# Performance work log

Hardware: AMD Instinct MI355X
Metric: run time of the kernel (lower is better)

The kernel has to match this reference:

```python
import jax, jax.numpy as jnp
import numpy as np

B, S, DIM = 2, 2048, 2048
N_HEADS, N_KV_HEADS, HEAD_DIM = 16, 4, 128
ROPE_THETA = 10000.0
N_REP = N_HEADS // N_KV_HEADS


def make_freq_cis(seq_len, head_dim, theta):
    # (seq_len, head_dim//2, 2, 2) rotation matrices [[cos,-sin],[sin,cos]]
    freqs = 1.0 / (theta ** (np.arange(0, head_dim, 2, dtype=np.float32) / head_dim))
    t = np.arange(seq_len, dtype=np.float32)
    ang = np.outer(t, freqs)  # [S, head_dim//2]
    cos, sin = np.cos(ang), np.sin(ang)
    row0 = np.stack([cos, -sin], axis=-1)
    row1 = np.stack([sin, cos], axis=-1)
    return jnp.asarray(np.stack([row0, row1], axis=-2))  # [S, hd/2, 2, 2]


def setup_inputs() -> dict:
    key = jax.random.key(0)
    ks = jax.random.split(key, 5)
    std = DIM ** -0.5
    x = jax.random.normal(ks[0], (B, S, DIM), dtype=jnp.float32)
    wq = jax.random.normal(ks[1], (N_HEADS * HEAD_DIM, DIM), dtype=jnp.float32) * std
    wk = jax.random.normal(ks[2], (N_KV_HEADS * HEAD_DIM, DIM), dtype=jnp.float32) * std
    wv = jax.random.normal(ks[3], (N_KV_HEADS * HEAD_DIM, DIM), dtype=jnp.float32) * std
    wo = jax.random.normal(ks[4], (DIM, N_HEADS * HEAD_DIM), dtype=jnp.float32) * std
    freq_cis = make_freq_cis(S, HEAD_DIM, ROPE_THETA)
    return {"x": x, "freq_cis": freq_cis, "wq": wq, "wk": wk, "wv": wv, "wo": wo}


def apply_rotary(xh, fc):
    # xh: [B,S,H,hd]; fc: [S, hd/2, 2, 2]
    b, s, h, hd = xh.shape
    xr = xh.reshape(b, s, h, hd // 2, 2)
    out = jnp.einsum('bshdj,sdij->bshdi', xr, fc)
    return out.reshape(b, s, h, hd)


def attention_fwd(x, freq_cis, wq, wk, wv, wo):
    b, s, _ = x.shape
    xq = (x @ wq.T).reshape(b, s, N_HEADS, HEAD_DIM)
    xk = (x @ wk.T).reshape(b, s, N_KV_HEADS, HEAD_DIM)
    xv = (x @ wv.T).reshape(b, s, N_KV_HEADS, HEAD_DIM)
    xq = apply_rotary(xq, freq_cis[:s])
    xk = apply_rotary(xk, freq_cis[:s])
    # GQA repeat_kv (repeat_interleave along head dim)
    xk = jnp.repeat(xk, N_REP, axis=2)
    xv = jnp.repeat(xv, N_REP, axis=2)
    scale = HEAD_DIM ** -0.5
    scores = jnp.einsum('bqhd,bkhd->bhqk', xq, xk) * scale
    causal = jnp.tril(jnp.ones((s, s), dtype=bool))
    scores = jnp.where(causal[None, None], scores, jnp.float32(-1e30))
    probs = jax.nn.softmax(scores, axis=-1)
    out = jnp.einsum('bhqk,bkhd->bqhd', probs, xv).reshape(b, s, N_HEADS * HEAD_DIM)
    return out @ wo.T


def reference(x, freq_cis, wq, wk, wv, wo):
    return attention_fwd(x, freq_cis, wq, wk, wv, wo)
```

## Files before the change

kernel.cpp:

```cpp
#include <hip/hip_runtime.h>

#define S_LEN 2048
#define N_B 2
#define N_H 16
#define N_KVH 4
#define HD 128
#define LDQ 2048
#define LDK 1024

typedef __bf16 bf16x8 __attribute__((ext_vector_type(8)));
typedef float f32x4 __attribute__((ext_vector_type(4)));
typedef float f32x16 __attribute__((ext_vector_type(16)));
typedef int v2i __attribute__((ext_vector_type(2)));

__device__ __forceinline__ float bf2f(unsigned short u){
  unsigned int x = ((unsigned int)u) << 16; float f;
  __builtin_memcpy(&f, &x, 4); return f;
}
__device__ __forceinline__ unsigned short f2bf(float f){
  unsigned int x; __builtin_memcpy(&x, &f, 4);
  unsigned int r = x + 0x7fff + ((x >> 16) & 1);
  return (unsigned short)(r >> 16);
}
__device__ __forceinline__ unsigned int cvt_pk_bf16(float lo, float hi){
  unsigned int u;
  asm("v_cvt_pk_bf16_f32 %0, %1, %2" : "=v"(u) : "v"(lo), "v"(hi));
  return u;
}
__device__ __forceinline__ void gload16(const void* g, void* l){
  __builtin_amdgcn_global_load_lds((const __attribute__((address_space(1))) void*)g,
                                   (__attribute__((address_space(3))) void*)l, 16, 0, 0);
}

__global__ void cast_all(const float* __restrict__ x,  const float* __restrict__ wq,
                         const float* __restrict__ wk, const float* __restrict__ wv,
                         const float* __restrict__ wo, unsigned short* __restrict__ xb,
                         unsigned short* __restrict__ wqb, unsigned short* __restrict__ wkb,
                         unsigned short* __restrict__ wvb, unsigned short* __restrict__ wob){
  int i = blockIdx.x * 256 + threadIdx.x;
  const float* in; unsigned short* out; int j;
  if (i < 1048576)      { in = x;  out = xb;  j = i; }
  else if (i < 1572864) { in = wq; out = wqb; j = i - 1048576; }
  else if (i < 1703936) { in = wk; out = wkb; j = i - 1572864; }
  else if (i < 1835008) { in = wv; out = wvb; j = i - 1703936; }
  else                  { in = wo; out = wob; j = i - 1835008; }
  const float4* p = (const float4*)in + (size_t)j * 2;
  float4 a = p[0], b = p[1];
  uint4 o;
  o.x = (unsigned)f2bf(a.x) | ((unsigned)f2bf(a.y) << 16);
  o.y = (unsigned)f2bf(a.z) | ((unsigned)f2bf(a.w) << 16);
  o.z = (unsigned)f2bf(b.x) | ((unsigned)f2bf(b.y) << 16);
  o.w = (unsigned)f2bf(b.z) | ((unsigned)f2bf(b.w) << 16);
  ((uint4*)out)[j] = o;
}

__global__ void rope_kernel(unsigned short* __restrict__ X, const float* __restrict__ FC,
                            int cpr_log2, int ld_log2, int n8){
  int i = blockIdx.x * 256 + threadIdx.x;
  if (i >= n8) return;
  int row = i >> cpr_log2;
  int col = (i & ((1 << cpr_log2) - 1)) << 3;
  size_t idx = ((size_t)row << ld_log2) + col;
  int s = row & (S_LEN - 1);
  int d = col & (HD - 1);
  uint4 v = *(const uint4*)(X + idx);
  unsigned short* pv = (unsigned short*)&v;
  const float4* f4 = (const float4*)FC + ((size_t)s * 64 + (d >> 1));
  uint4 ov; unsigned short* po = (unsigned short*)&ov;
#pragma unroll
  for (int p = 0; p < 4; p++){
    float4 f = f4[p];
    float e = bf2f(pv[2*p]), o = bf2f(pv[2*p+1]);
    po[2*p]   = f2bf(f.x * e + f.y * o);
    po[2*p+1] = f2bf(f.z * e + f.w * o);
  }
  *(uint4*)(X + idx) = ov;
}

__global__ void transpose_v(const unsigned short* __restrict__ V, unsigned short* __restrict__ Vt, int ld){
  __shared__ unsigned short tile[32][33];
  int t = threadIdx.x;
  int s0 = blockIdx.x * 32;
  int c0 = blockIdx.y * 32;
  int r = t >> 3, cg = (t & 7) * 4;
  uint2 in2 = *(const uint2*)(V + (size_t)(s0 + r) * ld + c0 + cg);
  unsigned short* pi = (unsigned short*)&in2;
  tile[r][cg+0] = pi[0]; tile[r][cg+1] = pi[1]; tile[r][cg+2] = pi[2]; tile[r][cg+3] = pi[3];
  __syncthreads();
  int b = s0 >> 11, sl = s0 & (S_LEN - 1);
  int kvh = c0 >> 7, dd0 = c0 & (HD - 1);
  int dd = t >> 3, sg = (t & 7) * 4;
  uint2 o2; unsigned short* po = (unsigned short*)&o2;
  po[0] = tile[sg+0][dd]; po[1] = tile[sg+1][dd]; po[2] = tile[sg+2][dd]; po[3] = tile[sg+3][dd];
  *(uint2*)(Vt + (size_t)((b * N_KVH + kvh) * HD + dd0 + dd) * S_LEN + sl + sg) = o2;
}

__device__ __forceinline__ void storeC(float* C, size_t idx, float v){ C[idx] = v; }
__device__ __forceinline__ void storeC(unsigned short* C, size_t idx, float v){ C[idx] = f2bf(v); }

template <typename OutT>
__global__ __launch_bounds__(256, 2) void gemm_nt(const unsigned short* __restrict__ A,
                                                  const unsigned short* __restrict__ Bm,
                                                  OutT* __restrict__ C,
                                                  int M, int N, int K, int nbn){
  extern __shared__ char smem[];
  char* sA = smem; char* sB = smem + 16384;
  int bid = blockIdx.x;
  bid = (bid & 7) * (gridDim.x >> 3) + (bid >> 3);
  int bn = bid % nbn, bm = bid / nbn;
  int row0 = bm * 128, col0 = bn * 128;
  int t = threadIdx.x; int w = t >> 6, l = t & 63;
  int lr = l & 15, lg = l >> 4;
  int srow = t >> 3;
  int sg = (t & 7) ^ (srow & 7);
  const unsigned short* agp = A + (size_t)(row0 + srow) * K + sg * 8;
  const unsigned short* bgp = Bm + (size_t)(col0 + srow) * K + sg * 8;
  int wr = w >> 1, wc = w & 1;
  f32x4 acc[4][4] = {};
  for (int k0 = 0; k0 < K; k0 += 64){
    __syncthreads();
#pragma unroll
    for (int i = 0; i < 4; i++){
      gload16(agp + (size_t)i * 32 * K + k0, sA + i * 4096 + w * 1024);
      gload16(bgp + (size_t)i * 32 * K + k0, sB + i * 4096 + w * 1024);
    }
    __syncthreads();
#pragma unroll
    for (int kk = 0; kk < 2; kk++){
      bf16x8 af[4], bfv[4];
#pragma unroll
      for (int m = 0; m < 4; m++){
        int row = wr * 64 + m * 16 + lr;
        int kg = kk * 4 + lg;
        af[m] = *(const bf16x8*)(sA + row * 128 + ((kg ^ (row & 7)) << 4));
      }
#pragma unroll
      for (int n = 0; n < 4; n++){
        int row = wc * 64 + n * 16 + lr;
        int kg = kk * 4 + lg;
        bfv[n] = *(const bf16x8*)(sB + row * 128 + ((kg ^ (row & 7)) << 4));
      }
#pragma unroll
      for (int m = 0; m < 4; m++)
#pragma unroll
        for (int n = 0; n < 4; n++)
          acc[m][n] = __builtin_amdgcn_mfma_f32_16x16x32_bf16(af[m], bfv[n], acc[m][n], 0, 0, 0);
    }
  }
#pragma unroll
  for (int m = 0; m < 4; m++)
#pragma unroll
    for (int n = 0; n < 4; n++)
#pragma unroll
      for (int r = 0; r < 4; r++){
        int rr = row0 + wr * 64 + m * 16 + lg * 4 + r;
        int cc = col0 + wc * 64 + n * 16 + lr;
        storeC(C, (size_t)rr * N + cc, acc[m][n][r]);
      }
}

template <typename OutT>
__global__ __launch_bounds__(512, 2) void gemm_tpl(const unsigned short* __restrict__ A,
                                                   const unsigned short* __restrict__ Bm,
                                                   OutT* __restrict__ C,
                                                   int M, int N, int K, int nbn){
  extern __shared__ char smem[];
  int bid = blockIdx.x;
  bid = (bid & 7) * (gridDim.x >> 3) + (bid >> 3);
  int bn = bid % nbn, bm = bid / nbn;
  int row0 = bm * 128, col0 = bn * 256;
  int t = threadIdx.x, w = t >> 6, l = t & 63;
  int lr = l & 15, lg = l >> 4;
  int wm = w >> 2, wn = w & 3;
  int srow = t >> 3;
  int sg = (t & 7) ^ (srow & 7);
  const unsigned short* agp = A + (size_t)(row0 + srow) * K + sg * 8;
  const unsigned short* bgp = Bm + (size_t)(col0 + srow) * K + sg * 8;
  int nk = K >> 6;
  f32x4 acc[4][4] = {};

#define TPL_STAGE_H1(j, s) do {                                                \
    char* base_ = smem + (s) * 49152;                                          \
    int k0_ = (j) << 6;                                                        \
    _Pragma("unroll")                                                          \
    for (int i_ = 0; i_ < 2; i_++)                                             \
      gload16(agp + (size_t)i_ * 64 * K + k0_, base_ + i_ * 8192 + w * 1024);  \
    gload16(bgp + k0_, base_ + 16384 + w * 1024);                              \
  } while(0)
#define TPL_STAGE_H2(j, s) do {                                                \
    char* base_ = smem + (s) * 49152;                                          \
    int k0_ = (j) << 6;                                                        \
    _Pragma("unroll")                                                          \
    for (int i_ = 1; i_ < 4; i_++)                                             \
      gload16(bgp + (size_t)i_ * 64 * K + k0_, base_ + 16384 + i_ * 8192 + w * 1024); \
  } while(0)

  TPL_STAGE_H1(0, 0); TPL_STAGE_H2(0, 0);
  TPL_STAGE_H1(1, 1); TPL_STAGE_H2(1, 1);
  int slot = 0;
  for (int j = 0; j < nk; j++){
    if (j + 1 < nk) asm volatile("s_waitcnt vmcnt(6)" ::: "memory");
    else            asm volatile("s_waitcnt vmcnt(0)" ::: "memory");
    __builtin_amdgcn_s_barrier();
    asm volatile("" ::: "memory");
    char* sA = smem + slot * 49152;
    char* sB = sA + 16384;
    int sn = slot + 2; if (sn >= 3) sn -= 3;
    {
      bf16x8 af[4], bfv[4];
#pragma unroll
      for (int m = 0; m < 4; m++){
        int row = wm * 64 + m * 16 + lr;
        af[m] = *(const bf16x8*)(sA + row * 128 + ((lg ^ (row & 7)) << 4));
      }
#pragma unroll
      for (int n = 0; n < 4; n++){
        int row = wn * 64 + n * 16 + lr;
        bfv[n] = *(const bf16x8*)(sB + row * 128 + ((lg ^ (row & 7)) << 4));
      }
      if (j + 2 < nk) TPL_STAGE_H1(j + 2, sn);
      __builtin_amdgcn_s_barrier();
      __builtin_amdgcn_s_setprio(1);
#pragma unroll
      for (int m = 0; m < 4; m++)
#pragma unroll
        for (int n = 0; n < 4; n++)
          acc[m][n] = __builtin_amdgcn_mfma_f32_16x16x32_bf16(af[m], bfv[n], acc[m][n], 0, 0, 0);
      __builtin_amdgcn_s_setprio(0);
      __builtin_amdgcn_s_barrier();
    }
    {
      bf16x8 af[4], bfv[4];
#pragma unroll
      for (int m = 0; m < 4; m++){
        int row = wm * 64 + m * 16 + lr;
        int kg = 4 + lg;
        af[m] = *(const bf16x8*)(sA + row * 128 + ((kg ^ (row & 7)) << 4));
      }
#pragma unroll
      for (int n = 0; n < 4; n++){
        int row = wn * 64 + n * 16 + lr;
        int kg = 4 + lg;
        bfv[n] = *(const bf16x8*)(sB + row * 128 + ((kg ^ (row & 7)) << 4));
      }
      if (j + 2 < nk) TPL_STAGE_H2(j + 2, sn);
      __builtin_amdgcn_s_barrier();
      __builtin_amdgcn_s_setprio(1);
#pragma unroll
      for (int m = 0; m < 4; m++)
#pragma unroll
        for (int n = 0; n < 4; n++)
          acc[m][n] = __builtin_amdgcn_mfma_f32_16x16x32_bf16(af[m], bfv[n], acc[m][n], 0, 0, 0);
      __builtin_amdgcn_s_setprio(0);
    }
    slot++; if (slot == 3) slot = 0;
  }
#undef TPL_STAGE_H1
#undef TPL_STAGE_H2
#pragma unroll
  for (int m = 0; m < 4; m++)
#pragma unroll
    for (int n = 0; n < 4; n++)
#pragma unroll
      for (int r = 0; r < 4; r++){
        int rr = row0 + wm * 64 + m * 16 + lg * 4 + r;
        int cc = col0 + wn * 64 + n * 16 + lr;
        storeC(C, (size_t)rr * N + cc, acc[m][n][r]);
      }
}

__global__ __launch_bounds__(256, 2) void attn_fwd(const unsigned short* __restrict__ Q,
                                                   const unsigned short* __restrict__ Kb,
                                                   const unsigned short* __restrict__ Vt,
                                                   unsigned short* __restrict__ P0,
                                                   unsigned short* __restrict__ P1,
                                                   float2* __restrict__ ML){
  extern __shared__ char smem[];
  const float SOFT_C = 0.088388347648318447f * 1.4426950408889634f;
  const float THR_RAW = 62.0f;
  int bid = blockIdx.x;
  bid = ((bid & 7) << 6) | (bid >> 3);
  int slot = bid & 15, h = (bid >> 4) & 15, b = bid >> 8;
  int p = slot & 7, half = slot >> 3;
  int kvh = h >> 2;
  int t = threadIdx.x, w = t >> 6, l = t & 63;
  int lq = l & 31, lh = l >> 5;
  unsigned short* Pout = half ? P1 : P0;
  float2* mlb = ML + half * (N_B * S_LEN * N_H);

  const unsigned short* kgp = Kb + ((size_t)(b * S_LEN) + (t & 63)) * LDK + kvh * HD + (t >> 6) * 8;
  const unsigned short* vgp = Vt + ((size_t)((b * N_KVH + kvh) * HD) + (t & 127)) * S_LEN + (t >> 7) * 8;

  for (int phase = 0; phase < 2; phase++){
    int qt = phase ? (15 - p) : p;
    int q_lane = qt * 128 + w * 32 + lq;
    const unsigned short* qbase = Q + ((size_t)(b * S_LEN + q_lane)) * LDQ + h * HD + lh * 8;
    bf16x8 qf[8];
#pragma unroll
    for (int ks = 0; ks < 8; ks++)
      qf[ks] = *(const bf16x8*)(qbase + ks * 16);

    f32x16 o_acc[4] = {};
    float m_run = -1e4f, l_run = 0.f;
    int t_begin = half ? (qt + 1) : 0;
    int t_end   = half ? (2 * qt + 2) : (qt + 1);

    {
      int k0 = t_begin * 64;
#pragma unroll
      for (int i = 0; i < 4; i++){
        gload16(kgp + (size_t)k0 * LDK + i * 32, smem + i * 4096 + t * 16);
        gload16(vgp + k0 + i * 16, smem + 16384 + i * 4096 + t * 16);
      }
    }
    __syncthreads();

    int cur = 0;
    for (int tix = t_begin; tix < t_end; tix++){
      int k0 = tix * 64;
      char* kb = smem + (cur << 15);
      if (tix + 1 < t_end){
        char* nb = smem + ((cur ^ 1) << 15);
        int nk0 = k0 + 64;
#pragma unroll
        for (int i = 0; i < 4; i++){
          gload16(kgp + (size_t)nk0 * LDK + i * 32, nb + i * 4096 + t * 16);
          gload16(vgp + nk0 + i * 16, nb + 16384 + i * 4096 + t * 16);
        }
      }

      f32x16 sc[2] = {};
      __builtin_amdgcn_s_setprio(1);
#pragma unroll
      for (int ks = 0; ks < 8; ks++){
#pragma unroll
        for (int n = 0; n < 2; n++){
          bf16x8 kf = *(const bf16x8*)(kb + (ks * 2 + lh) * 1024 + n * 512 + lq * 16);
          sc[n] = __builtin_amdgcn_mfma_f32_32x32x16_bf16(kf, qf[ks], sc[n], 0, 0, 0);
        }
      }
      __builtin_amdgcn_s_setprio(0);
      if (tix >= 2 * qt){
#pragma unroll
        for (int n = 0; n < 2; n++)
#pragma unroll
          for (int reg = 0; reg < 16; reg++){
            int kv = k0 + n * 32 + (reg & 3) + 8 * (reg >> 2) + 4 * lh;
            if (kv > q_lane) sc[n][reg] = -1e30f;
          }
      }
      float tmax = sc[0][0];
#pragma unroll
      for (int n = 0; n < 2; n++)
#pragma unroll
        for (int reg = 0; reg < 16; reg++) tmax = fmaxf(tmax, sc[n][reg]);
      tmax = fmaxf(tmax, __shfl_xor(tmax, 32));
      if (!__all(tmax - m_run <= THR_RAW)){
        float nm = fmaxf(m_run, tmax);
        float rs = exp2f((m_run - nm) * SOFT_C);
        m_run = nm;
        l_run *= rs;
#pragma unroll
        for (int n = 0; n < 4; n++)
#pragma unroll
          for (int j = 0; j < 16; j++) o_acc[n][j] *= rs;
      }
      float lsum = 0.f;
#pragma unroll
      for (int n = 0; n < 2; n++)
#pragma unroll
        for (int reg = 0; reg < 16; reg++){
          float pv = exp2f((sc[n][reg] - m_run) * SOFT_C);
          sc[n][reg] = pv;
          lsum += pv;
        }
      lsum += __shfl_xor(lsum, 32);
      l_run += lsum;

      bf16x8 pb[4];
#pragma unroll
      for (int ks = 0; ks < 4; ks++){
        int n = ks >> 1;
        int R0 = (2 * ks) & 3, R1 = (2 * ks + 1) & 3;
        unsigned int WA0 = cvt_pk_bf16(sc[n][4 * R0 + 0], sc[n][4 * R0 + 1]);
        unsigned int WA1 = cvt_pk_bf16(sc[n][4 * R0 + 2], sc[n][4 * R0 + 3]);
        unsigned int WB0 = cvt_pk_bf16(sc[n][4 * R1 + 0], sc[n][4 * R1 + 1]);
        unsigned int WB1 = cvt_pk_bf16(sc[n][4 * R1 + 2], sc[n][4 * R1 + 3]);
        v2i s0 = __builtin_amdgcn_permlane32_swap((int)WA0, (int)WB0, false, false);
        v2i s1 = __builtin_amdgcn_permlane32_swap((int)WA1, (int)WB1, false, false);
        unsigned int pu[4] = {(unsigned int)s0.x, (unsigned int)s1.x,
                              (unsigned int)s0.y, (unsigned int)s1.y};
        pb[ks] = *(bf16x8*)pu;
      }
      __builtin_amdgcn_s_setprio(1);
#pragma unroll
      for (int n = 0; n < 4; n++){
#pragma unroll
        for (int ks = 0; ks < 4; ks++){
          bf16x8 vf = *(const bf16x8*)(kb + 16384 + (ks * 2 + lh) * 2048 + n * 512 + lq * 16);
          o_acc[n] = __builtin_amdgcn_mfma_f32_32x32x16_bf16(vf, pb[ks], o_acc[n], 0, 0, 0);
        }
      }
      __builtin_amdgcn_s_setprio(0);
      __syncthreads();
      cur ^= 1;
    }
    unsigned short* ob = Pout + ((size_t)(b * S_LEN + q_lane)) * LDQ + h * HD + 4 * lh;
#pragma unroll
    for (int n = 0; n < 4; n++)
#pragma unroll
      for (int g = 0; g < 4; g++){
        unsigned int u0 = cvt_pk_bf16(o_acc[n][4 * g + 0], o_acc[n][4 * g + 1]);
        unsigned int u1 = cvt_pk_bf16(o_acc[n][4 * g + 2], o_acc[n][4 * g + 3]);
        uint2 o2; o2.x = u0; o2.y = u1;
        *(uint2*)(ob + n * 32 + g * 8) = o2;
      }
    if (lh == 0)
      mlb[(size_t)(b * S_LEN + q_lane) * N_H + h] = make_float2(m_run, l_run);
  }
}

__global__ void attn_merge(unsigned short* __restrict__ P0, const unsigned short* __restrict__ P1,
                           const float2* __restrict__ ML){
  const float SOFT_C = 0.088388347648318447f * 1.4426950408889634f;
  int tid = blockIdx.x * 256 + threadIdx.x;
  float2 a = ML[tid >> 4];
  float2 c = ML[(N_B * S_LEN * N_H) + (tid >> 4)];
  float m = fmaxf(a.x, c.x);
  float w0 = exp2f((a.x - m) * SOFT_C) * a.y;
  float w1 = exp2f((c.x - m) * SOFT_C) * c.y;
  float inv = 1.0f / (w0 + w1);
  float s0 = exp2f((a.x - m) * SOFT_C) * inv;
  float s1 = exp2f((c.x - m) * SOFT_C) * inv;
  uint4 u0 = *(const uint4*)(P0 + (size_t)tid * 8);
  uint4 u1 = *(const uint4*)(P1 + (size_t)tid * 8);
  unsigned short* q0 = (unsigned short*)&u0;
  unsigned short* q1 = (unsigned short*)&u1;
  uint4 o;
  unsigned int* po = (unsigned int*)&o;
#pragma unroll
  for (int j = 0; j < 4; j++){
    float lo = s0 * bf2f(q0[2*j])   + s1 * bf2f(q1[2*j]);
    float hi = s0 * bf2f(q0[2*j+1]) + s1 * bf2f(q1[2*j+1]);
    po[j] = cvt_pk_bf16(lo, hi);
  }
  *(uint4*)(P0 + (size_t)tid * 8) = o;
}

extern "C" void kernel_launch(void* const* d_in, const int* in_sizes, int n_in,
                              void* d_out, int out_size, void* d_ws, size_t ws_size,
                              hipStream_t stream) {
  const float* x  = (const float*)d_in[0];
  const float* fc = (const float*)d_in[1];
  const float* wq = (const float*)d_in[2];
  const float* wk = (const float*)d_in[3];
  const float* wv = (const float*)d_in[4];
  const float* wo = (const float*)d_in[5];
  float* out = (float*)d_out;

  char* ws = (char*)d_ws;
  unsigned short* xb  = (unsigned short*)(ws);
  unsigned short* wqb = (unsigned short*)(ws + 16777216);
  unsigned short* wkb = (unsigned short*)(ws + 25165824);
  unsigned short* wvb = (unsigned short*)(ws + 27262976);
  unsigned short* wob = (unsigned short*)(ws + 29360128);
  unsigned short* qb_ = (unsigned short*)(ws + 37748736);
  unsigned short* kvb = (unsigned short*)(ws + 54525952);
  unsigned short* vtb = (unsigned short*)(ws + 62914560);
  unsigned short* ab_ = (unsigned short*)(ws + 67108864);
  unsigned short* p1_ = xb;
  float2*         ml_ = (float2*)wqb;

  cast_all<<<9216, 256, 0, stream>>>(x, wq, wk, wv, wo, xb, wqb, wkb, wvb, wob);

  gemm_tpl<unsigned short><<<256, 512, 147456, stream>>>(xb, wqb, qb_, 4096, 2048, 2048, 8);
  gemm_nt<unsigned short><<<256, 256, 32768, stream>>>(xb, wkb, kvb, 4096, 1024, 2048, 8);

  rope_kernel<<<4096, 256, 0, stream>>>(qb_, fc, 8, 11, 1048576);
  rope_kernel<<<1024, 256, 0, stream>>>(kvb, fc, 6, 10, 262144);

  transpose_v<<<dim3(128, 16), 256, 0, stream>>>(kvb + 512, vtb, 1024);

  attn_fwd<<<512, 256, 65536, stream>>>(qb_, kvb, vtb, ab_, p1_, ml_);
  attn_merge<<<4096, 256, 0, stream>>>(ab_, p1_, ml_);

  gemm_tpl<float><<<256, 512, 147456, stream>>>(ab_, wob, out, 4096, 2048, 2048, 8);
}
```

Before: 216.4 us.

## Fuse RoPE into GEMM epilogues and swizzle K/V shared-memory layout in attention

Removes the two standalone RoPE kernels by applying the rotation in the Q and KV projection GEMM epilogues. Each lane gets its pair partner with a lane shuffle and reads the rotation coefficients from freq_cis. Rotating the fp32 accumulator before the bf16 store also drops one rounding step. Separately, the attention kernel now loads K and V tiles into shared memory row-major with an XOR swizzle, replacing the previous interleaved layout, to cut LDS bank conflicts and improve global load coalescing. The epilogue gains extra global loads of freq_cis per element and a shuffle, which may slow the GEMM tail.

```diff
diff --git a/kernel.cpp b/kernel.cpp
--- a/kernel.cpp
+++ b/kernel.cpp
@@ -54,29 +54,6 @@
   ((uint4*)out)[j] = o;
 }
 
-__global__ void rope_kernel(unsigned short* __restrict__ X, const float* __restrict__ FC,
-                            int cpr_log2, int ld_log2, int n8){
-  int i = blockIdx.x * 256 + threadIdx.x;
-  if (i >= n8) return;
-  int row = i >> cpr_log2;
-  int col = (i & ((1 << cpr_log2) - 1)) << 3;
-  size_t idx = ((size_t)row << ld_log2) + col;
-  int s = row & (S_LEN - 1);
-  int d = col & (HD - 1);
-  uint4 v = *(const uint4*)(X + idx);
-  unsigned short* pv = (unsigned short*)&v;
-  const float4* f4 = (const float4*)FC + ((size_t)s * 64 + (d >> 1));
-  uint4 ov; unsigned short* po = (unsigned short*)&ov;
-#pragma unroll
-  for (int p = 0; p < 4; p++){
-    float4 f = f4[p];
-    float e = bf2f(pv[2*p]), o = bf2f(pv[2*p+1]);
-    po[2*p]   = f2bf(f.x * e + f.y * o);
-    po[2*p+1] = f2bf(f.z * e + f.w * o);
-  }
-  *(uint4*)(X + idx) = ov;
-}
-
 __global__ void transpose_v(const unsigned short* __restrict__ V, unsigned short* __restrict__ Vt, int ld){
   __shared__ unsigned short tile[32][33];
   int t = threadIdx.x;
@@ -98,11 +75,18 @@
 __device__ __forceinline__ void storeC(float* C, size_t idx, float v){ C[idx] = v; }
 __device__ __forceinline__ void storeC(unsigned short* C, size_t idx, float v){ C[idx] = f2bf(v); }
 
+__device__ __forceinline__ float rope_elem(float v, int odd, int s, int d, const float* FC){
+  float partner = __shfl_xor(v, 1);
+  float4 f = *((const float4*)FC + ((s << 6) + (d >> 1)));
+  return odd ? (f.z * partner + f.w * v) : (f.x * v + f.y * partner);
+}
+
 template <typename OutT>
 __global__ __launch_bounds__(256, 2) void gemm_nt(const unsigned short* __restrict__ A,
                                                   const unsigned short* __restrict__ Bm,
                                                   OutT* __restrict__ C,
-                                                  int M, int N, int K, int nbn){
+                                                  int M, int N, int K, int nbn,
+                                                  const float* __restrict__ FC, int rope_cols){
   extern __shared__ char smem[];
   char* sA = smem; char* sB = smem + 16384;
   int bid = blockIdx.x;
@@ -147,6 +131,7 @@
           acc[m][n] = __builtin_amdgcn_mfma_f32_16x16x32_bf16(af[m], bfv[n], acc[m][n], 0, 0, 0);
     }
   }
+  bool do_rope = (col0 < rope_cols);
 #pragma unroll
   for (int m = 0; m < 4; m++)
 #pragma unroll
@@ -155,7 +140,9 @@
       for (int r = 0; r < 4; r++){
         int rr = row0 + wr * 64 + m * 16 + lg * 4 + r;
         int cc = col0 + wc * 64 + n * 16 + lr;
-        storeC(C, (size_t)rr * N + cc, acc[m][n][r]);
+        float v = acc[m][n][r];
+        if (do_rope) v = rope_elem(v, lr & 1, rr & (S_LEN - 1), cc & (HD - 1), FC);
+        storeC(C, (size_t)rr * N + cc, v);
       }
 }
 
@@ -163,7 +150,8 @@
 __global__ __launch_bounds__(512, 2) void gemm_tpl(const unsigned short* __restrict__ A,
                                                    const unsigned short* __restrict__ Bm,
                                                    OutT* __restrict__ C,
-                                                   int M, int N, int K, int nbn){
+                                                   int M, int N, int K, int nbn,
+                                                   const float* __restrict__ FC, int rope_cols){
   extern __shared__ char smem[];
   int bid = blockIdx.x;
   bid = (bid & 7) * (gridDim.x >> 3) + (bid >> 3);
@@ -257,6 +245,7 @@
   }
 #undef TPL_STAGE_H1
 #undef TPL_STAGE_H2
+  bool do_rope = (col0 < rope_cols);
 #pragma unroll
   for (int m = 0; m < 4; m++)
 #pragma unroll
@@ -265,7 +254,9 @@
       for (int r = 0; r < 4; r++){
         int rr = row0 + wm * 64 + m * 16 + lg * 4 + r;
         int cc = col0 + wn * 64 + n * 16 + lr;
-        storeC(C, (size_t)rr * N + cc, acc[m][n][r]);
+        float v = acc[m][n][r];
+        if (do_rope) v = rope_elem(v, lr & 1, rr & (S_LEN - 1), cc & (HD - 1), FC);
+        storeC(C, (size_t)rr * N + cc, v);
       }
 }
 
@@ -288,8 +279,10 @@
   unsigned short* Pout = half ? P1 : P0;
   float2* mlb = ML + half * (N_B * S_LEN * N_H);
 
-  const unsigned short* kgp = Kb + ((size_t)(b * S_LEN) + (t & 63)) * LDK + kvh * HD + (t >> 6) * 8;
-  const unsigned short* vgp = Vt + ((size_t)((b * N_KVH + kvh) * HD) + (t & 127)) * S_LEN + (t >> 7) * 8;
+  int gA = (t & 15) ^ (t >> 4);
+  const unsigned short* kgp = Kb + ((size_t)(b * S_LEN) + (t >> 4)) * LDK + kvh * HD + gA * 8;
+  int gV = (t & 7) ^ ((t >> 3) & 7);
+  const unsigned short* vgp = Vt + ((size_t)((b * N_KVH + kvh) * HD) + (t >> 3)) * S_LEN + gV * 8;
 
   for (int phase = 0; phase < 2; phase++){
     int qt = phase ? (15 - p) : p;
@@ -305,28 +298,29 @@
     int t_begin = half ? (qt + 1) : 0;
     int t_end   = half ? (2 * qt + 2) : (qt + 1);
 
-    {
-      int k0 = t_begin * 64;
-#pragma unroll
-      for (int i = 0; i < 4; i++){
-        gload16(kgp + (size_t)k0 * LDK + i * 32, smem + i * 4096 + t * 16);
-        gload16(vgp + k0 + i * 16, smem + 16384 + i * 4096 + t * 16);
-      }
-    }
+    int pk0 = t_begin * 64;
+#pragma unroll
+    for (int m = 0; m < 4; m++)
+      gload16(kgp + (size_t)(pk0 + m * 16) * LDK, smem + m * 4096 + w * 1024);
+#pragma unroll
+    for (int i = 0; i < 4; i++)
+      gload16(vgp + (size_t)i * 32 * S_LEN + pk0, smem + 16384 + i * 4096 + w * 1024);
     __syncthreads();
 
     int cur = 0;
     for (int tix = t_begin; tix < t_end; tix++){
       int k0 = tix * 64;
-      char* kb = smem + (cur << 15);
+      char* sK = smem + (cur << 15);
+      char* sV = sK + 16384;
       if (tix + 1 < t_end){
         char* nb = smem + ((cur ^ 1) << 15);
         int nk0 = k0 + 64;
 #pragma unroll
-        for (int i = 0; i < 4; i++){
-          gload16(kgp + (size_t)nk0 * LDK + i * 32, nb + i * 4096 + t * 16);
-          gload16(vgp + nk0 + i * 16, nb + 16384 + i * 4096 + t * 16);
-        }
+        for (int m = 0; m < 4; m++)
+          gload16(kgp + (size_t)(nk0 + m * 16) * LDK, nb + m * 4096 + w * 1024);
+#pragma unroll
+        for (int i = 0; i < 4; i++)
+          gload16(vgp + (size_t)i * 32 * S_LEN + nk0, nb + 16384 + i * 4096 + w * 1024);
       }
 
       f32x16 sc[2] = {};
@@ -335,7 +329,9 @@
       for (int ks = 0; ks < 8; ks++){
 #pragma unroll
         for (int n = 0; n < 2; n++){
-          bf16x8 kf = *(const bf16x8*)(kb + (ks * 2 + lh) * 1024 + n * 512 + lq * 16);
+          int row = n * 32 + lq;
+          int pg = (ks * 2 + lh) ^ (row & 15);
+          bf16x8 kf = *(const bf16x8*)(sK + row * 256 + pg * 16);
           sc[n] = __builtin_amdgcn_mfma_f32_32x32x16_bf16(kf, qf[ks], sc[n], 0, 0, 0);
         }
       }
@@ -397,7 +393,9 @@
       for (int n = 0; n < 4; n++){
 #pragma unroll
         for (int ks = 0; ks < 4; ks++){
-          bf16x8 vf = *(const bf16x8*)(kb + 16384 + (ks * 2 + lh) * 2048 + n * 512 + lq * 16);
+          int row = n * 32 + lq;
+          int pg = (ks * 2 + lh) ^ (row & 7);
+          bf16x8 vf = *(const bf16x8*)(sV + row * 128 + pg * 16);
           o_acc[n] = __builtin_amdgcn_mfma_f32_32x32x16_bf16(vf, pb[ks], o_acc[n], 0, 0, 0);
         }
       }
@@ -473,16 +471,13 @@
 
   cast_all<<<9216, 256, 0, stream>>>(x, wq, wk, wv, wo, xb, wqb, wkb, wvb, wob);
 
-  gemm_tpl<unsigned short><<<256, 512, 147456, stream>>>(xb, wqb, qb_, 4096, 2048, 2048, 8);
-  gemm_nt<unsigned short><<<256, 256, 32768, stream>>>(xb, wkb, kvb, 4096, 1024, 2048, 8);
-
-  rope_kernel<<<4096, 256, 0, stream>>>(qb_, fc, 8, 11, 1048576);
-  rope_kernel<<<1024, 256, 0, stream>>>(kvb, fc, 6, 10, 262144);
+  gemm_tpl<unsigned short><<<256, 512, 147456, stream>>>(xb, wqb, qb_, 4096, 2048, 2048, 8, fc, 2048);
+  gemm_nt<unsigned short><<<256, 256, 32768, stream>>>(xb, wkb, kvb, 4096, 1024, 2048, 8, fc, 512);
 
   transpose_v<<<dim3(128, 16), 256, 0, stream>>>(kvb + 512, vtb, 1024);
 
   attn_fwd<<<512, 256, 65536, stream>>>(qb_, kvb, vtb, ab_, p1_, ml_);
   attn_merge<<<4096, 256, 0, stream>>>(ab_, p1_, ml_);
 
-  gemm_tpl<float><<<256, 512, 147456, stream>>>(ab_, wob, out, 4096, 2048, 2048, 8);
-}
+  gemm_tpl<float><<<256, 512, 147456, stream>>>(ab_, wob, out, 4096, 2048, 2048, 8, fc, 0);
+}
```

After: 245.6 us. 13.5% more time.
